# Optimization experiments

Hardware: AMD Instinct MI355X
Metric: run time of the kernel (lower is better)

## Reference

```python
import jax, jax.numpy as jnp
import numpy as np

N_NODES = 21
N_ACTIONS = 256
NODE_FEAT = 128


def _gcn_norm(edge_index, n):
    # Dense normalized adjacency mirroring PyG gcn_norm with add_self_loops=True.
    row, col = edge_index[0], edge_index[1]
    A = jnp.zeros((n, n), dtype=jnp.float32).at[row, col].add(1.0)
    A = A + jnp.eye(n, dtype=jnp.float32)  # self loops appended with weight 1
    deg = A.sum(axis=0)                    # scatter-add of edge weights by col
    dinv = jnp.where(deg > 0, 1.0 / jnp.sqrt(deg), 0.0)
    # out[row] += dinv[row] * dinv[col] * x[col]  ->  A_norm = D^-1/2 A D^-1/2
    return dinv[:, None] * A * dinv[None, :]


def setup_inputs() -> dict:
    key = jax.random.key(0)
    ks = jax.random.split(key, 12)
    B = 65536
    state = jax.random.normal(ks[0], (B, N_NODES, NODE_FEAT), dtype=jnp.float32)
    edge_index = jax.random.randint(ks[1], (2, 128), 0, N_NODES, dtype=jnp.int32)

    def lin(k, fan_in, fan_out):
        s = 1.0 / np.sqrt(fan_in)
        kw, kb = jax.random.split(k)
        W = jax.random.uniform(kw, (fan_in, fan_out), jnp.float32, -s, s)
        b = jax.random.uniform(kb, (fan_out,), jnp.float32, -s, s)
        return W, b

    W1, b1 = lin(ks[2], NODE_FEAT, 21)
    W2, b2 = lin(ks[3], 21, 21)
    Wf1, bf1 = lin(ks[4], 441, 512)
    Wf2, bf2 = lin(ks[5], 512, 512)
    Wf3, bf3 = lin(ks[6], 512, N_ACTIONS)
    return {"state": state, "edge_index": edge_index,
            "W1": W1, "b1": b1, "W2": W2, "b2": b2,
            "Wf1": Wf1, "bf1": bf1, "Wf2": Wf2, "bf2": bf2,
            "Wf3": Wf3, "bf3": bf3}


def reference(state, edge_index, W1, b1, W2, b2, Wf1, bf1, Wf2, bf2, Wf3, bf3):
    A = _gcn_norm(edge_index, N_NODES)                      # [21, 21]
    # GCNConv 1: A_norm @ (X W1) + b1   (no nonlinearity between GCN layers)
    h = jnp.einsum('bnf,fh->bnh', state, W1)                # [B, 21, 21]
    h = jnp.einsum('ij,bjh->bih', A, h) + b1
    # GCNConv 2
    h = jnp.einsum('bnf,fh->bnh', h, W2)
    h = jnp.einsum('ij,bjh->bih', A, h) + b2                # [B, 21, 21]
    v = h.reshape(h.shape[0], -1)[0]                        # x.view(B,-1)[0] -> [441]
    x = jax.nn.relu(v @ Wf1 + bf1)
    x = jax.nn.relu(x @ Wf2 + bf2)
    x = jax.nn.relu(x @ Wf3 + bf3)                          # [n_actions]
    return x
```

## Files before the change

### kernel.cpp

```cpp
#include <hip/hip_runtime.h>
#include <math.h>

#define APAD 28
#define W1PAD 132

#define WS_ACC1 0
#define WS_ACC2 512
#define WS_ACC3 1024

__device__ unsigned g_arrive[64 * 16];
__device__ unsigned g_go;
__device__ unsigned g_zr;
__device__ unsigned g_cnt;

__device__ __forceinline__ float agent_load(const float* p) {
    return __hip_atomic_load(p, __ATOMIC_RELAXED, __HIP_MEMORY_SCOPE_AGENT);
}
__device__ __forceinline__ void agent_store(float* p, float v) {
    __hip_atomic_store(p, v, __ATOMIC_RELAXED, __HIP_MEMORY_SCOPE_AGENT);
}
__device__ __forceinline__ unsigned flag_load(const unsigned* p) {
    return __hip_atomic_load(p, __ATOMIC_RELAXED, __HIP_MEMORY_SCOPE_AGENT);
}
__device__ __forceinline__ void flag_store(unsigned* p, unsigned v) {
    __hip_atomic_store(p, v, __ATOMIC_RELAXED, __HIP_MEMORY_SCOPE_AGENT);
}
__device__ __forceinline__ float agent_fadd(float* p, float v) {
    return __hip_atomic_fetch_add(p, v, __ATOMIC_RELAXED, __HIP_MEMORY_SCOPE_AGENT);
}

__device__ __forceinline__ void lds_barrier() {
    asm volatile("s_waitcnt lgkmcnt(0)\n\ts_barrier" ::: "memory");
}

__device__ __forceinline__ void grid_barrier(int blk, unsigned phase) {
    __syncthreads();
    if (blk == 0) {
        if (threadIdx.x > 0 && threadIdx.x < 64) {
            while (flag_load(&g_arrive[threadIdx.x * 16]) < phase)
                __builtin_amdgcn_s_sleep(1);
        }
        if (threadIdx.x == 0) flag_store(&g_go, phase);
    } else {
        if (threadIdx.x == 0) {
            flag_store(&g_arrive[blk * 16], phase);
            while (flag_load(&g_go) < phase)
                __builtin_amdgcn_s_sleep(1);
        }
    }
    __syncthreads();
}

__global__ __launch_bounds__(512) void fused_kernel(
    const float* __restrict__ state,
    const int*   __restrict__ edge_index,
    const float* __restrict__ W1,
    const float* __restrict__ b1,
    const float* __restrict__ W2,
    const float* __restrict__ b2,
    const float* __restrict__ Wf1,
    const float* __restrict__ bf1,
    const float* __restrict__ Wf2,
    const float* __restrict__ bf2,
    const float* __restrict__ Wf3,
    const float* __restrict__ bf3,
    float* __restrict__ ws,
    float* __restrict__ out)
{
    const int b = blockIdx.x;
    const int t = threadIdx.x;

    const bool is_gcn = (b < 21);
    const bool do_fc2 = (b >= 21 && b < 37);
    const bool do_fc3 = (b >= 37 && b < 45);

    __shared__ float sA[21 * APAD];
    __shared__ float sX[21 * W1PAD];
    __shared__ float sW1T[21 * W1PAD];
    __shared__ float sW2T[21 * APAD];
    __shared__ float sT[21 * APAD];
    __shared__ float sG[21 * APAD];
    __shared__ float sv[441];
    __shared__ float sdeg[21];
    __shared__ float sb1[21], sb2[21];
    __shared__ float x1s[32], x2s[64];
    __shared__ unsigned sflag;

    float wf1v[21];
    if (is_gcn) {
        #pragma unroll
        for (int i = 0; i < 21; ++i) wf1v[i] = Wf1[(size_t)(21 * b + i) * 512 + t];
    }
    float wf2v[32];
    float rbf1 = 0.0f;
    if (do_fc2) {
        #pragma unroll
        for (int i = 0; i < 32; ++i) wf2v[i] = Wf2[(size_t)(32 * (b - 21) + i) * 512 + t];
        if (t < 32) rbf1 = bf1[32 * (b - 21) + t];
    }
    float wf3v[64];
    float rbf2 = 0.0f;
    if (do_fc3) {
        if (t < 256) {
            #pragma unroll
            for (int i = 0; i < 64; ++i) wf3v[i] = Wf3[(size_t)(64 * (b - 37) + i) * 256 + t];
        }
        if (t < 64) rbf2 = bf2[64 * (b - 37) + t];
    }
    const float rbf3 = bf3[t & 255];

    if (b == 63) {
        agent_store(&ws[WS_ACC1 + t], 0.0f);
        agent_store(&ws[WS_ACC2 + t], 0.0f);
        if (t < 256) agent_store(&ws[WS_ACC3 + t], 0.0f);
        __syncthreads();
        if (t == 0) flag_store(&g_zr, 1u);
    }

    if (is_gcn) {
        for (int i = t; i < 21 * APAD; i += 512) {
            sA[i] = 0.0f; sW2T[i] = 0.0f; sT[i] = 0.0f; sG[i] = 0.0f;
        }
        if (t < 21) { sdeg[t] = 1.0f; sb1[t] = b1[t]; sb2[t] = b2[t]; }
        {
            const float4* src4 = (const float4*)state;
            for (int i = t; i < 672; i += 512) {
                int n = i >> 5, fc = i & 31;
                ((float4*)&sX[n * W1PAD])[fc] = src4[i];
            }
        }
        for (int i = t; i < 2688; i += 512) {
            int f = i / 21, k = i - f * 21;
            sW1T[k * W1PAD + f] = W1[i];
        }
        for (int i = t; i < 441; i += 512) {
            int f = i / 21, k = i - f * 21;
            sW2T[k * APAD + f] = W2[i];
        }
        int er = 0, ec = 0;
        if (t < 128) { er = edge_index[t]; ec = edge_index[128 + t]; }
        lds_barrier();

        if (t < 128) {
            atomicAdd(&sA[er * APAD + ec], 1.0f);
            atomicAdd(&sdeg[ec], 1.0f);
        }
        if (t < 21) atomicAdd(&sA[t * APAD + t], 1.0f);
        if (t < 441) {
            int n = t / 21, k = t - n * 21;
            const float4* x4 = (const float4*)&sX[n * W1PAD];
            const float4* w4 = (const float4*)&sW1T[k * W1PAD];
            float s = 0.0f;
            #pragma unroll
            for (int fc = 0; fc < 32; ++fc) {
                float4 a = x4[fc], ww = w4[fc];
                s += a.x * ww.x; s += a.y * ww.y; s += a.z * ww.z; s += a.w * ww.w;
            }
            sT[k * APAD + n] = s;
        }
        lds_barrier();

        if (t < 441) {
            int r = t / 21, c = t - r * 21;
            float dr = 1.0f / sqrtf(sdeg[r]);
            float dc = 1.0f / sqrtf(sdeg[c]);
            sA[r * APAD + c] = dr * sA[r * APAD + c] * dc;
        }
        lds_barrier();

        if (t < 441) {
            int r = t / 21, k = t - r * 21;
            const float4* a4 = (const float4*)&sA[r * APAD];
            const float4* h4 = (const float4*)&sT[k * APAD];
            float s = sb1[k];
            #pragma unroll
            for (int jc = 0; jc < 6; ++jc) {
                float4 a = a4[jc], h = h4[jc];
                s += a.x * h.x; s += a.y * h.y; s += a.z * h.z; s += a.w * h.w;
            }
            sG[r * APAD + k] = s;
        }
        lds_barrier();

        if (t < 441) {
            int n = t / 21, k = t - n * 21;
            const float4* g4 = (const float4*)&sG[n * APAD];
            const float4* w4 = (const float4*)&sW2T[k * APAD];
            float s = 0.0f;
            #pragma unroll
            for (int jc = 0; jc < 6; ++jc) {
                float4 g = g4[jc], ww = w4[jc];
                s += g.x * ww.x; s += g.y * ww.y; s += g.z * ww.z; s += g.w * ww.w;
            }
            sT[k * APAD + n] = s;
        }
        lds_barrier();

        if (t < 441) {
            int r = t / 21, k = t - r * 21;
            const float4* a4 = (const float4*)&sA[r * APAD];
            const float4* h4 = (const float4*)&sT[k * APAD];
            float s = sb2[k];
            #pragma unroll
            for (int jc = 0; jc < 6; ++jc) {
                float4 a = a4[jc], h = h4[jc];
                s += a.x * h.x; s += a.y * h.y; s += a.z * h.z; s += a.w * h.w;
            }
            sv[t] = s;
        }
        lds_barrier();

        if (t == 0) {
            while (flag_load(&g_zr) == 0u) __builtin_amdgcn_s_sleep(1);
        }
        __syncthreads();

        {
            float s = 0.0f;
            #pragma unroll
            for (int r = 0; r < 21; ++r) s += sv[21 * b + r] * wf1v[r];
            agent_fadd(&ws[WS_ACC1 + t], s);
        }
    }

    grid_barrier(b, 1);

    if (do_fc2) {
        if (t < 32)
            x1s[t] = fmaxf(agent_load(&ws[WS_ACC1 + 32 * (b - 21) + t]) + rbf1, 0.0f);
        lds_barrier();
        float s = 0.0f;
        #pragma unroll
        for (int j = 0; j < 32; ++j) s += x1s[j] * wf2v[j];
        agent_fadd(&ws[WS_ACC2 + t], s);
    }

    grid_barrier(b, 2);

    if (do_fc3) {
        if (t < 64)
            x2s[t] = fmaxf(agent_load(&ws[WS_ACC2 + 64 * (b - 37) + t]) + rbf2, 0.0f);
        lds_barrier();
        if (t < 256) {
            float s = 0.0f;
            #pragma unroll
            for (int j = 0; j < 64; ++j) s += x2s[j] * wf3v[j];
            agent_fadd(&ws[WS_ACC3 + t], s);
        }
    }

    __syncthreads();
    if (t == 0) {
        unsigned prev = __hip_atomic_fetch_add(&g_cnt, 1u, __ATOMIC_RELAXED,
                                               __HIP_MEMORY_SCOPE_AGENT);
        sflag = (prev == 63u) ? 1u : 0u;
    }
    __syncthreads();
    if (sflag) {
        if (t < 256) {
            float a = agent_load(&ws[WS_ACC3 + t]) + rbf3;
            out[t] = fmaxf(a, 0.0f);
        }
        if (t >= 256 && t < 320) flag_store(&g_arrive[(t - 256) * 16], 0u);
        if (t == 320) flag_store(&g_go, 0u);
        if (t == 321) flag_store(&g_zr, 0u);
        if (t == 322) flag_store(&g_cnt, 0u);
    }
}

extern "C" void kernel_launch(void* const* d_in, const int* in_sizes, int n_in,
                              void* d_out, int out_size, void* d_ws, size_t ws_size,
                              hipStream_t stream)
{
    const float* state      = (const float*)d_in[0];
    const int*   edge_index = (const int*)  d_in[1];
    const float* W1  = (const float*)d_in[2];
    const float* b1  = (const float*)d_in[3];
    const float* W2  = (const float*)d_in[4];
    const float* b2  = (const float*)d_in[5];
    const float* Wf1 = (const float*)d_in[6];
    const float* bf1 = (const float*)d_in[7];
    const float* Wf2 = (const float*)d_in[8];
    const float* bf2 = (const float*)d_in[9];
    const float* Wf3 = (const float*)d_in[10];
    const float* bf3 = (const float*)d_in[11];

    float* ws  = (float*)d_ws;
    float* out = (float*)d_out;

    fused_kernel<<<64, 512, 0, stream>>>(state, edge_index, W1, b1, W2, b2,
                                         Wf1, bf1, Wf2, bf2, Wf3, bf3, ws, out);
}
```

Measured before the change: 16.32 us.

## Replace grid barriers with per-stage counters and trim grid to active blocks

Drops the two full grid barriers and synchronizes each stage with its own counter. FC2 blocks wait until all 21 GCN blocks have bumped a counter, and FC3 blocks wait until all 16 FC2 blocks have. The launch shrinks from 64 to 45 blocks so idle blocks no longer take part, and each GCN block now computes only the one row of the final GCN product it needs. This removes barrier round-trips and idle-block participation, but it relies on relaxed atomics for ordering, which risks memory-visibility races between the accumulation adds and the counter bumps.

```diff
diff --git a/kernel.cpp b/kernel.cpp
--- a/kernel.cpp
+++ b/kernel.cpp
@@ -8,9 +8,9 @@
 #define WS_ACC2 512
 #define WS_ACC3 1024
 
-__device__ unsigned g_arrive[64 * 16];
-__device__ unsigned g_go;
 __device__ unsigned g_zr;
+__device__ unsigned g_d1;
+__device__ unsigned g_d2;
 __device__ unsigned g_cnt;
 
 __device__ __forceinline__ float agent_load(const float* p) {
@@ -25,30 +25,16 @@
 __device__ __forceinline__ void flag_store(unsigned* p, unsigned v) {
     __hip_atomic_store(p, v, __ATOMIC_RELAXED, __HIP_MEMORY_SCOPE_AGENT);
 }
+__device__ __forceinline__ void flag_bump(unsigned* p, unsigned* out_prev) {
+    *out_prev = __hip_atomic_fetch_add(p, 1u, __ATOMIC_RELAXED,
+                                       __HIP_MEMORY_SCOPE_AGENT);
+}
 __device__ __forceinline__ float agent_fadd(float* p, float v) {
     return __hip_atomic_fetch_add(p, v, __ATOMIC_RELAXED, __HIP_MEMORY_SCOPE_AGENT);
 }
 
 __device__ __forceinline__ void lds_barrier() {
     asm volatile("s_waitcnt lgkmcnt(0)\n\ts_barrier" ::: "memory");
-}
-
-__device__ __forceinline__ void grid_barrier(int blk, unsigned phase) {
-    __syncthreads();
-    if (blk == 0) {
-        if (threadIdx.x > 0 && threadIdx.x < 64) {
-            while (flag_load(&g_arrive[threadIdx.x * 16]) < phase)
-                __builtin_amdgcn_s_sleep(1);
-        }
-        if (threadIdx.x == 0) flag_store(&g_go, phase);
-    } else {
-        if (threadIdx.x == 0) {
-            flag_store(&g_arrive[blk * 16], phase);
-            while (flag_load(&g_go) < phase)
-                __builtin_amdgcn_s_sleep(1);
-        }
-    }
-    __syncthreads();
 }
 
 __global__ __launch_bounds__(512) void fused_kernel(
@@ -70,9 +56,91 @@
     const int b = blockIdx.x;
     const int t = threadIdx.x;
 
-    const bool is_gcn = (b < 21);
-    const bool do_fc2 = (b >= 21 && b < 37);
-    const bool do_fc3 = (b >= 37 && b < 45);
+    if (b >= 37) {
+        if (b == 44) {
+            agent_store(&ws[WS_ACC1 + t], 0.0f);
+            agent_store(&ws[WS_ACC2 + t], 0.0f);
+            if (t < 256) agent_store(&ws[WS_ACC3 + t], 0.0f);
+            __syncthreads();
+            if (t == 0) flag_store(&g_zr, 1u);
+        }
+
+        const int r0 = 64 * (b - 37);
+        float wf3v[64];
+        if (t < 256) {
+            #pragma unroll
+            for (int i = 0; i < 64; ++i)
+                wf3v[i] = Wf3[(size_t)(r0 + i) * 256 + t];
+        }
+        const float rbf2 = (t < 64) ? bf2[r0 + t] : 0.0f;
+        const float rbf3 = bf3[t & 255];
+
+        __shared__ float x2s[64];
+        __shared__ unsigned sflag;
+
+        if (t == 0) {
+            while (flag_load(&g_d2) < 16u) __builtin_amdgcn_s_sleep(1);
+        }
+        __syncthreads();
+
+        if (t < 64)
+            x2s[t] = fmaxf(agent_load(&ws[WS_ACC2 + r0 + t]) + rbf2, 0.0f);
+        lds_barrier();
+        if (t < 256) {
+            float s = 0.0f;
+            #pragma unroll
+            for (int j = 0; j < 64; ++j) s += x2s[j] * wf3v[j];
+            agent_fadd(&ws[WS_ACC3 + t], s);
+        }
+
+        __syncthreads();
+        if (t == 0) {
+            unsigned prev; flag_bump(&g_cnt, &prev);
+            sflag = (prev == 7u) ? 1u : 0u;
+        }
+        __syncthreads();
+        if (sflag) {
+            if (t < 256) {
+                float a = agent_load(&ws[WS_ACC3 + t]) + rbf3;
+                out[t] = fmaxf(a, 0.0f);
+            }
+            if (t == 256) flag_store(&g_zr, 0u);
+            if (t == 257) flag_store(&g_d1, 0u);
+            if (t == 258) flag_store(&g_d2, 0u);
+            if (t == 259) flag_store(&g_cnt, 0u);
+        }
+        return;
+    }
+
+    if (b >= 21) {
+        const int r0 = 32 * (b - 21);
+        float wf2v[32];
+        #pragma unroll
+        for (int i = 0; i < 32; ++i)
+            wf2v[i] = Wf2[(size_t)(r0 + i) * 512 + t];
+        const float rbf1 = (t < 32) ? bf1[r0 + t] : 0.0f;
+
+        __shared__ float x1s[32];
+
+        if (t == 0) {
+            while (flag_load(&g_d1) < 21u) __builtin_amdgcn_s_sleep(1);
+        }
+        __syncthreads();
+
+        if (t < 32)
+            x1s[t] = fmaxf(agent_load(&ws[WS_ACC1 + r0 + t]) + rbf1, 0.0f);
+        lds_barrier();
+        {
+            float s = 0.0f;
+            #pragma unroll
+            for (int j = 0; j < 32; ++j) s += x1s[j] * wf2v[j];
+            agent_fadd(&ws[WS_ACC2 + t], s);
+        }
+
+        __syncthreads();
+        if (t == 0) { unsigned prev; flag_bump(&g_d2, &prev); }
+        return;
+    }
 
     __shared__ float sA[21 * APAD];
     __shared__ float sX[21 * W1PAD];
@@ -80,192 +148,119 @@
     __shared__ float sW2T[21 * APAD];
     __shared__ float sT[21 * APAD];
     __shared__ float sG[21 * APAD];
-    __shared__ float sv[441];
+    __shared__ float sv[21];
     __shared__ float sdeg[21];
     __shared__ float sb1[21], sb2[21];
-    __shared__ float x1s[32], x2s[64];
-    __shared__ unsigned sflag;
+
+    for (int i = t; i < 21 * APAD; i += 512) {
+        sA[i] = 0.0f; sW2T[i] = 0.0f; sT[i] = 0.0f; sG[i] = 0.0f;
+    }
+    if (t < 21) { sdeg[t] = 1.0f; sb1[t] = b1[t]; sb2[t] = b2[t]; }
+    {
+        const float4* src4 = (const float4*)state;
+        for (int i = t; i < 672; i += 512) {
+            int n = i >> 5, fc = i & 31;
+            ((float4*)&sX[n * W1PAD])[fc] = src4[i];
+        }
+    }
+    for (int i = t; i < 2688; i += 512) {
+        int f = i / 21, k = i - f * 21;
+        sW1T[k * W1PAD + f] = W1[i];
+    }
+    for (int i = t; i < 441; i += 512) {
+        int f = i / 21, k = i - f * 21;
+        sW2T[k * APAD + f] = W2[i];
+    }
+    int er = 0, ec = 0;
+    if (t < 128) { er = edge_index[t]; ec = edge_index[128 + t]; }
 
     float wf1v[21];
-    if (is_gcn) {
-        #pragma unroll
-        for (int i = 0; i < 21; ++i) wf1v[i] = Wf1[(size_t)(21 * b + i) * 512 + t];
-    }
-    float wf2v[32];
-    float rbf1 = 0.0f;
-    if (do_fc2) {
-        #pragma unroll
-        for (int i = 0; i < 32; ++i) wf2v[i] = Wf2[(size_t)(32 * (b - 21) + i) * 512 + t];
-        if (t < 32) rbf1 = bf1[32 * (b - 21) + t];
-    }
-    float wf3v[64];
-    float rbf2 = 0.0f;
-    if (do_fc3) {
-        if (t < 256) {
-            #pragma unroll
-            for (int i = 0; i < 64; ++i) wf3v[i] = Wf3[(size_t)(64 * (b - 37) + i) * 256 + t];
-        }
-        if (t < 64) rbf2 = bf2[64 * (b - 37) + t];
-    }
-    const float rbf3 = bf3[t & 255];
-
-    if (b == 63) {
-        agent_store(&ws[WS_ACC1 + t], 0.0f);
-        agent_store(&ws[WS_ACC2 + t], 0.0f);
-        if (t < 256) agent_store(&ws[WS_ACC3 + t], 0.0f);
-        __syncthreads();
-        if (t == 0) flag_store(&g_zr, 1u);
-    }
-
-    if (is_gcn) {
-        for (int i = t; i < 21 * APAD; i += 512) {
-            sA[i] = 0.0f; sW2T[i] = 0.0f; sT[i] = 0.0f; sG[i] = 0.0f;
-        }
-        if (t < 21) { sdeg[t] = 1.0f; sb1[t] = b1[t]; sb2[t] = b2[t]; }
-        {
-            const float4* src4 = (const float4*)state;
-            for (int i = t; i < 672; i += 512) {
-                int n = i >> 5, fc = i & 31;
-                ((float4*)&sX[n * W1PAD])[fc] = src4[i];
-            }
-        }
-        for (int i = t; i < 2688; i += 512) {
-            int f = i / 21, k = i - f * 21;
-            sW1T[k * W1PAD + f] = W1[i];
-        }
-        for (int i = t; i < 441; i += 512) {
-            int f = i / 21, k = i - f * 21;
-            sW2T[k * APAD + f] = W2[i];
-        }
-        int er = 0, ec = 0;
-        if (t < 128) { er = edge_index[t]; ec = edge_index[128 + t]; }
-        lds_barrier();
-
-        if (t < 128) {
-            atomicAdd(&sA[er * APAD + ec], 1.0f);
-            atomicAdd(&sdeg[ec], 1.0f);
-        }
-        if (t < 21) atomicAdd(&sA[t * APAD + t], 1.0f);
-        if (t < 441) {
-            int n = t / 21, k = t - n * 21;
-            const float4* x4 = (const float4*)&sX[n * W1PAD];
-            const float4* w4 = (const float4*)&sW1T[k * W1PAD];
-            float s = 0.0f;
-            #pragma unroll
-            for (int fc = 0; fc < 32; ++fc) {
-                float4 a = x4[fc], ww = w4[fc];
-                s += a.x * ww.x; s += a.y * ww.y; s += a.z * ww.z; s += a.w * ww.w;
-            }
-            sT[k * APAD + n] = s;
-        }
-        lds_barrier();
-
-        if (t < 441) {
-            int r = t / 21, c = t - r * 21;
-            float dr = 1.0f / sqrtf(sdeg[r]);
-            float dc = 1.0f / sqrtf(sdeg[c]);
-            sA[r * APAD + c] = dr * sA[r * APAD + c] * dc;
-        }
-        lds_barrier();
-
-        if (t < 441) {
-            int r = t / 21, k = t - r * 21;
-            const float4* a4 = (const float4*)&sA[r * APAD];
-            const float4* h4 = (const float4*)&sT[k * APAD];
-            float s = sb1[k];
-            #pragma unroll
-            for (int jc = 0; jc < 6; ++jc) {
-                float4 a = a4[jc], h = h4[jc];
-                s += a.x * h.x; s += a.y * h.y; s += a.z * h.z; s += a.w * h.w;
-            }
-            sG[r * APAD + k] = s;
-        }
-        lds_barrier();
-
-        if (t < 441) {
-            int n = t / 21, k = t - n * 21;
-            const float4* g4 = (const float4*)&sG[n * APAD];
-            const float4* w4 = (const float4*)&sW2T[k * APAD];
-            float s = 0.0f;
-            #pragma unroll
-            for (int jc = 0; jc < 6; ++jc) {
-                float4 g = g4[jc], ww = w4[jc];
-                s += g.x * ww.x; s += g.y * ww.y; s += g.z * ww.z; s += g.w * ww.w;
-            }
-            sT[k * APAD + n] = s;
-        }
-        lds_barrier();
-
-        if (t < 441) {
-            int r = t / 21, k = t - r * 21;
-            const float4* a4 = (const float4*)&sA[r * APAD];
-            const float4* h4 = (const float4*)&sT[k * APAD];
-            float s = sb2[k];
-            #pragma unroll
-            for (int jc = 0; jc < 6; ++jc) {
-                float4 a = a4[jc], h = h4[jc];
-                s += a.x * h.x; s += a.y * h.y; s += a.z * h.z; s += a.w * h.w;
-            }
-            sv[t] = s;
-        }
-        lds_barrier();
-
-        if (t == 0) {
-            while (flag_load(&g_zr) == 0u) __builtin_amdgcn_s_sleep(1);
-        }
-        __syncthreads();
-
-        {
-            float s = 0.0f;
-            #pragma unroll
-            for (int r = 0; r < 21; ++r) s += sv[21 * b + r] * wf1v[r];
-            agent_fadd(&ws[WS_ACC1 + t], s);
-        }
-    }
-
-    grid_barrier(b, 1);
-
-    if (do_fc2) {
-        if (t < 32)
-            x1s[t] = fmaxf(agent_load(&ws[WS_ACC1 + 32 * (b - 21) + t]) + rbf1, 0.0f);
-        lds_barrier();
+    #pragma unroll
+    for (int i = 0; i < 21; ++i) wf1v[i] = Wf1[(size_t)(21 * b + i) * 512 + t];
+
+    lds_barrier();
+
+    if (t < 128) {
+        atomicAdd(&sA[er * APAD + ec], 1.0f);
+        atomicAdd(&sdeg[ec], 1.0f);
+    }
+    if (t < 21) atomicAdd(&sA[t * APAD + t], 1.0f);
+    if (t < 441) {
+        int n = t / 21, k = t - n * 21;
+        const float4* x4 = (const float4*)&sX[n * W1PAD];
+        const float4* w4 = (const float4*)&sW1T[k * W1PAD];
         float s = 0.0f;
         #pragma unroll
-        for (int j = 0; j < 32; ++j) s += x1s[j] * wf2v[j];
-        agent_fadd(&ws[WS_ACC2 + t], s);
-    }
-
-    grid_barrier(b, 2);
-
-    if (do_fc3) {
-        if (t < 64)
-            x2s[t] = fmaxf(agent_load(&ws[WS_ACC2 + 64 * (b - 37) + t]) + rbf2, 0.0f);
-        lds_barrier();
-        if (t < 256) {
-            float s = 0.0f;
-            #pragma unroll
-            for (int j = 0; j < 64; ++j) s += x2s[j] * wf3v[j];
-            agent_fadd(&ws[WS_ACC3 + t], s);
-        }
+        for (int fc = 0; fc < 32; ++fc) {
+            float4 a = x4[fc], ww = w4[fc];
+            s += a.x * ww.x; s += a.y * ww.y; s += a.z * ww.z; s += a.w * ww.w;
+        }
+        sT[k * APAD + n] = s;
+    }
+    lds_barrier();
+
+    if (t < 441) {
+        int r = t / 21, c = t - r * 21;
+        float dr = 1.0f / sqrtf(sdeg[r]);
+        float dc = 1.0f / sqrtf(sdeg[c]);
+        sA[r * APAD + c] = dr * sA[r * APAD + c] * dc;
+    }
+    lds_barrier();
+
+    if (t < 441) {
+        int r = t / 21, k = t - r * 21;
+        const float4* a4 = (const float4*)&sA[r * APAD];
+        const float4* h4 = (const float4*)&sT[k * APAD];
+        float s = sb1[k];
+        #pragma unroll
+        for (int jc = 0; jc < 6; ++jc) {
+            float4 a = a4[jc], h = h4[jc];
+            s += a.x * h.x; s += a.y * h.y; s += a.z * h.z; s += a.w * h.w;
+        }
+        sG[r * APAD + k] = s;
+    }
+    lds_barrier();
+
+    if (t < 441) {
+        int n = t / 21, k = t - n * 21;
+        const float4* g4 = (const float4*)&sG[n * APAD];
+        const float4* w4 = (const float4*)&sW2T[k * APAD];
+        float s = 0.0f;
+        #pragma unroll
+        for (int jc = 0; jc < 6; ++jc) {
+            float4 g = g4[jc], ww = w4[jc];
+            s += g.x * ww.x; s += g.y * ww.y; s += g.z * ww.z; s += g.w * ww.w;
+        }
+        sT[k * APAD + n] = s;
+    }
+    lds_barrier();
+
+    if (t < 21) {
+        const int k = t;
+        const float4* a4 = (const float4*)&sA[b * APAD];
+        const float4* h4 = (const float4*)&sT[k * APAD];
+        float s = sb2[k];
+        #pragma unroll
+        for (int jc = 0; jc < 6; ++jc) {
+            float4 a = a4[jc], h = h4[jc];
+            s += a.x * h.x; s += a.y * h.y; s += a.z * h.z; s += a.w * h.w;
+        }
+        sv[k] = s;
+    }
+    if (t == 448) {
+        while (flag_load(&g_zr) == 0u) __builtin_amdgcn_s_sleep(1);
+    }
+    lds_barrier();
+
+    {
+        float s = 0.0f;
+        #pragma unroll
+        for (int r = 0; r < 21; ++r) s += sv[r] * wf1v[r];
+        agent_fadd(&ws[WS_ACC1 + t], s);
     }
 
     __syncthreads();
-    if (t == 0) {
-        unsigned prev = __hip_atomic_fetch_add(&g_cnt, 1u, __ATOMIC_RELAXED,
-                                               __HIP_MEMORY_SCOPE_AGENT);
-        sflag = (prev == 63u) ? 1u : 0u;
-    }
-    __syncthreads();
-    if (sflag) {
-        if (t < 256) {
-            float a = agent_load(&ws[WS_ACC3 + t]) + rbf3;
-            out[t] = fmaxf(a, 0.0f);
-        }
-        if (t >= 256 && t < 320) flag_store(&g_arrive[(t - 256) * 16], 0u);
-        if (t == 320) flag_store(&g_go, 0u);
-        if (t == 321) flag_store(&g_zr, 0u);
-        if (t == 322) flag_store(&g_cnt, 0u);
-    }
+    if (t == 0) { unsigned prev; flag_bump(&g_d1, &prev); }
 }
 
 extern "C" void kernel_launch(void* const* d_in, const int* in_sizes, int n_in,
@@ -288,6 +283,6 @@
     float* ws  = (float*)d_ws;
     float* out = (float*)d_out;
 
-    fused_kernel<<<64, 512, 0, stream>>>(state, edge_index, W1, b1, W2, b2,
+    fused_kernel<<<45, 512, 0, stream>>>(state, edge_index, W1, b1, W2, b2,
                                          Wf1, bf1, Wf2, bf2, Wf3, bf3, ws, out);
 }
```

New measurement: 16.40 us. About the same (+0.5%).
